# Kernel optimization log

Hardware: AMD Instinct MI355X
Metric: run time of the kernel (lower is better)

The kernel has to match this reference:

```python
import jax, jax.numpy as jnp
import numpy as np
import math

HIDDEN = 256
HEADS = 8
HEAD_DIM = HIDDEN // HEADS
SCALE = math.sqrt(HEAD_DIM)


def setup_inputs() -> dict:
    key = jax.random.key(0)
    ks = jax.random.split(key, 10)
    B, N = 2, 4096
    x = jax.random.normal(ks[0], (B, N, HIDDEN), dtype=jnp.float32)
    pos = jax.random.normal(ks[1], (B, N, 3), dtype=jnp.float32)
    s = 1.0 / math.sqrt(HIDDEN)
    Wq = jax.random.normal(ks[2], (HIDDEN, HIDDEN), dtype=jnp.float32) * s
    bq = jnp.zeros((HIDDEN,), dtype=jnp.float32)
    Wk = jax.random.normal(ks[3], (HIDDEN, HIDDEN), dtype=jnp.float32) * s
    bk = jnp.zeros((HIDDEN,), dtype=jnp.float32)
    Wv = jax.random.normal(ks[4], (HIDDEN, HIDDEN), dtype=jnp.float32) * s
    bv = jnp.zeros((HIDDEN,), dtype=jnp.float32)
    Wo = jax.random.normal(ks[5], (HIDDEN, HIDDEN), dtype=jnp.float32) * s
    bo = jnp.zeros((HIDDEN,), dtype=jnp.float32)
    return {"x": x, "pos": pos, "Wq": Wq, "bq": bq, "Wk": Wk, "bk": bk,
            "Wv": Wv, "bv": bv, "Wo": Wo, "bo": bo}


def _pairwise_dist(pos):
    # Euclidean cdist via the norm trick; clip for numerical safety.
    sq = jnp.sum(pos * pos, axis=-1)  # [B, N]
    d2 = sq[:, :, None] + sq[:, None, :] - 2.0 * jnp.einsum('bic,bjc->bij', pos, pos)
    return jnp.sqrt(jnp.maximum(d2, 0.0))  # [B, N, N]


def reference(x, pos, Wq, bq, Wk, bk, Wv, bv, Wo, bo):
    B, N, _ = x.shape
    # projections -> [B, H, N, Dh]
    def split_heads(t):
        return t.reshape(B, N, HEADS, HEAD_DIM).transpose(0, 2, 1, 3)
    q = split_heads(x @ Wq.T + bq)
    k = split_heads(x @ Wk.T + bk)
    v = split_heads(x @ Wv.T + bv)
    scores = jnp.einsum('bhid,bhjd->bhij', q, k) / SCALE
    dist_bias = -_pairwise_dist(pos) / 10.0  # [B, N, N]
    scores = scores + dist_bias[:, None, :, :]
    attn = jax.nn.softmax(scores, axis=-1)
    out = jnp.einsum('bhij,bhjd->bhid', attn, v)
    out = out.transpose(0, 2, 1, 3).reshape(B, N, HIDDEN)
    return out @ Wo.T + bo
```

## Files before the change

### kernel.cpp

```cpp
#include <hip/hip_runtime.h>

#define BATCH 2
#define SEQ   4096
#define HID   256
#define NHEAD 8
#define DH    32

typedef __attribute__((ext_vector_type(8))) _Float16 half8;
typedef __attribute__((ext_vector_type(4))) _Float16 half4;
typedef __attribute__((ext_vector_type(4))) float    f32x4;

__global__ void cvt_f32_f16(const float* __restrict__ src,
                            _Float16* __restrict__ dst, int n) {
    int i = (blockIdx.x * blockDim.x + threadIdx.x) * 4;
    if (i >= n) return;
    f32x4 v = *reinterpret_cast<const f32x4*>(src + i);
    half4 h;
#pragma unroll
    for (int c = 0; c < 4; ++c) h[c] = (_Float16)v[c];
    *reinterpret_cast<half4*>(dst + i) = h;
}

__global__ __launch_bounds__(256) void qkv_proj(
    const _Float16* __restrict__ xh, const _Float16* __restrict__ Wh,
    const float* __restrict__ bq, const float* __restrict__ bk,
    const float* __restrict__ bv,
    _Float16* __restrict__ Qh, _Float16* __restrict__ Kh,
    _Float16* __restrict__ Vt)
{
    const int z   = blockIdx.z;
    const int m0  = blockIdx.x * 64;
    const int n0  = blockIdx.y * 64;
    const int tid = threadIdx.x;
    const int w   = tid >> 6, lane = tid & 63;
    const int lr  = lane & 15, lg = lane >> 4;
    const int wr  = (w >> 1) * 32, wc = (w & 1) * 32;

    const _Float16* Wp = Wh + (size_t)z * HID * HID;
    const float* bias = (z == 0) ? bq : (z == 1) ? bk : bv;

    f32x4 acc[2][2] = {};
    const int ar = m0 + wr + lr;
    const int br = n0 + wc + lr;
#pragma unroll
    for (int ks = 0; ks < 8; ++ks) {
        const int ko = ks * 32 + lg * 8;
        half8 a0 = *reinterpret_cast<const half8*>(xh + (size_t)ar * HID + ko);
        half8 a1 = *reinterpret_cast<const half8*>(xh + (size_t)(ar + 16) * HID + ko);
        half8 b0 = *reinterpret_cast<const half8*>(Wp + (size_t)br * HID + ko);
        half8 b1 = *reinterpret_cast<const half8*>(Wp + (size_t)(br + 16) * HID + ko);
        acc[0][0] = __builtin_amdgcn_mfma_f32_16x16x32_f16(a0, b0, acc[0][0], 0, 0, 0);
        acc[0][1] = __builtin_amdgcn_mfma_f32_16x16x32_f16(a0, b1, acc[0][1], 0, 0, 0);
        acc[1][0] = __builtin_amdgcn_mfma_f32_16x16x32_f16(a1, b0, acc[1][0], 0, 0, 0);
        acc[1][1] = __builtin_amdgcn_mfma_f32_16x16x32_f16(a1, b1, acc[1][1], 0, 0, 0);
    }
#pragma unroll
    for (int mf = 0; mf < 2; ++mf)
#pragma unroll
    for (int nf = 0; nf < 2; ++nf)
#pragma unroll
    for (int r = 0; r < 4; ++r) {
        const int m  = m0 + wr + mf * 16 + lg * 4 + r;
        const int o  = n0 + wc + nf * 16 + lr;
        const int bb = m >> 12, nn = m & (SEQ - 1);
        const int hh = o >> 5,  dd = o & (DH - 1);
        float v = acc[mf][nf][r] + bias[o];
        if (z == 0) {
            Qh[(((size_t)(bb * NHEAD + hh) * SEQ) + nn) * DH + dd] =
                (_Float16)(v * 0.17677669529663687f);
        } else if (z == 1) {
            Kh[(((size_t)(bb * NHEAD + hh) * SEQ) + nn) * DH + dd] = (_Float16)v;
        } else {
            Vt[(((size_t)(bb * NHEAD + hh) * DH) + dd) * SEQ + nn] = (_Float16)v;
        }
    }
}

__global__ __launch_bounds__(512) void attn_kernel(
    const _Float16* __restrict__ Qh, const _Float16* __restrict__ Kh,
    const _Float16* __restrict__ Vt, const float* __restrict__ pos,
    _Float16* __restrict__ AO)
{
    __shared__ __align__(16) float pi[32][4];
    __shared__ __align__(16) float pj[64][4];
    __shared__ __align__(16) float sbias[32][68];
    __shared__ __align__(16) _Float16 Pl[NHEAD][2048];

    const int b   = blockIdx.y;
    const int i0  = blockIdx.x * 32;
    const int tid = threadIdx.x;
    const int h   = tid >> 6;
    const int lane = tid & 63;
    const int lr  = lane & 15, lg = lane >> 4;

    if (tid < 32) {
        const float* p = pos + (size_t)(b * SEQ + i0 + tid) * 3;
        float x = p[0], y = p[1], zz = p[2];
        pi[tid][0] = x; pi[tid][1] = y; pi[tid][2] = zz;
        pi[tid][3] = x * x + y * y + zz * zz;
    }

    const _Float16* Qbase = Qh + ((size_t)(b * NHEAD + h) * SEQ + i0) * DH;
    const _Float16* Kbase = Kh + (size_t)(b * NHEAD + h) * SEQ * DH;
    const _Float16* Vbase = Vt + (size_t)(b * NHEAD + h) * DH * SEQ;

    const half8 aq0 = *reinterpret_cast<const half8*>(Qbase + (size_t)lr * DH + lg * 8);
    const half8 aq1 = *reinterpret_cast<const half8*>(Qbase + (size_t)(16 + lr) * DH + lg * 8);

    f32x4 acc[2][2] = {};
    float mrun[2][4], lrun[2][4];
#pragma unroll
    for (int mf = 0; mf < 2; ++mf)
#pragma unroll
    for (int r = 0; r < 4; ++r) { mrun[mf][r] = -__builtin_inff(); lrun[mf][r] = 0.f; }

    char* Pbytes = (char*)&Pl[h][0];

    for (int jt = 0; jt < SEQ / 64; ++jt) {
        const int j0 = jt * 64;
        __syncthreads();
        if (tid < 64) {
            const float* p = pos + (size_t)(b * SEQ + j0 + tid) * 3;
            float x = p[0], y = p[1], zz = p[2];
            pj[tid][0] = x; pj[tid][1] = y; pj[tid][2] = zz;
            pj[tid][3] = x * x + y * y + zz * zz;
        }
        __syncthreads();
        {
            const int row = tid >> 4, c0 = (tid & 15) * 4;
            const float xi = pi[row][0], yi = pi[row][1], zi = pi[row][2], si = pi[row][3];
            f32x4 bb;
#pragma unroll
            for (int c = 0; c < 4; ++c) {
                const int col = c0 + c;
                float dot = xi * pj[col][0] + yi * pj[col][1] + zi * pj[col][2];
                float d2  = si + pj[col][3] - 2.f * dot;
                bb[c] = -0.1f * sqrtf(fmaxf(d2, 0.f));
            }
            *reinterpret_cast<f32x4*>(&sbias[row][c0]) = bb;
        }
        __syncthreads();

        half8 bk8[4];
#pragma unroll
        for (int cf = 0; cf < 4; ++cf)
            bk8[cf] = *reinterpret_cast<const half8*>(
                Kbase + (size_t)(j0 + cf * 16 + lr) * DH + lg * 8);
        f32x4 s[2][4];
#pragma unroll
        for (int mf = 0; mf < 2; ++mf)
#pragma unroll
        for (int cf = 0; cf < 4; ++cf) {
            f32x4 zero = {};
            s[mf][cf] = __builtin_amdgcn_mfma_f32_16x16x32_f16(
                mf ? aq1 : aq0, bk8[cf], zero, 0, 0, 0);
        }

#pragma unroll
        for (int mf = 0; mf < 2; ++mf)
#pragma unroll
        for (int r = 0; r < 4; ++r) {
            const int row = mf * 16 + lg * 4 + r;
            float v[4];
#pragma unroll
            for (int c = 0; c < 4; ++c) v[c] = s[mf][c][r] + sbias[row][c * 16 + lr];
            float tmax = fmaxf(fmaxf(v[0], v[1]), fmaxf(v[2], v[3]));
#pragma unroll
            for (int msk = 8; msk >= 1; msk >>= 1)
                tmax = fmaxf(tmax, __shfl_xor(tmax, msk, 64));
            const float mold = mrun[mf][r];
            const float mnew = fmaxf(mold, tmax);
            const float alpha = __expf(mold - mnew);
            float rsum = 0.f;
#pragma unroll
            for (int c = 0; c < 4; ++c) { v[c] = __expf(v[c] - mnew); rsum += v[c]; }
#pragma unroll
            for (int msk = 8; msk >= 1; msk >>= 1)
                rsum += __shfl_xor(rsum, msk, 64);
            lrun[mf][r] = lrun[mf][r] * alpha + rsum;
            mrun[mf][r] = mnew;
            acc[mf][0][r] *= alpha;
            acc[mf][1][r] *= alpha;
#pragma unroll
            for (int c = 0; c < 4; ++c) {
                const int col = c * 16 + lr;
                const int off = (row * 128 + col * 2) ^ ((row & 7) << 4);
                *reinterpret_cast<_Float16*>(Pbytes + off) = (_Float16)v[c];
            }
        }

#pragma unroll
        for (int ks = 0; ks < 2; ++ks) {
            half8 bv0 = *reinterpret_cast<const half8*>(
                Vbase + (size_t)lr * SEQ + j0 + ks * 32 + lg * 8);
            half8 bv1 = *reinterpret_cast<const half8*>(
                Vbase + (size_t)(16 + lr) * SEQ + j0 + ks * 32 + lg * 8);
#pragma unroll
            for (int mf = 0; mf < 2; ++mf) {
                const int prow = mf * 16 + lr;
                const int poff = (prow * 128 + (ks * 32 + lg * 8) * 2) ^ ((prow & 7) << 4);
                half8 pa = *reinterpret_cast<const half8*>(Pbytes + poff);
                acc[mf][0] = __builtin_amdgcn_mfma_f32_16x16x32_f16(pa, bv0, acc[mf][0], 0, 0, 0);
                acc[mf][1] = __builtin_amdgcn_mfma_f32_16x16x32_f16(pa, bv1, acc[mf][1], 0, 0, 0);
            }
        }
    }

#pragma unroll
    for (int mf = 0; mf < 2; ++mf)
#pragma unroll
    for (int r = 0; r < 4; ++r) {
        const float inv = 1.f / lrun[mf][r];
        const int row = mf * 16 + lg * 4 + r;
#pragma unroll
        for (int df = 0; df < 2; ++df) {
            AO[((size_t)(b * SEQ + i0 + row)) * HID + h * DH + df * 16 + lr] =
                (_Float16)(acc[mf][df][r] * inv);
        }
    }
}

__global__ __launch_bounds__(256) void out_proj(
    const _Float16* __restrict__ AO, const _Float16* __restrict__ Woh,
    const float* __restrict__ bo, float* __restrict__ out)
{
    const int m0  = blockIdx.x * 64;
    const int n0  = blockIdx.y * 64;
    const int tid = threadIdx.x;
    const int w   = tid >> 6, lane = tid & 63;
    const int lr  = lane & 15, lg = lane >> 4;
    const int wr  = (w >> 1) * 32, wc = (w & 1) * 32;

    f32x4 acc[2][2] = {};
    const int ar = m0 + wr + lr;
    const int br = n0 + wc + lr;
#pragma unroll
    for (int ks = 0; ks < 8; ++ks) {
        const int ko = ks * 32 + lg * 8;
        half8 a0 = *reinterpret_cast<const half8*>(AO + (size_t)ar * HID + ko);
        half8 a1 = *reinterpret_cast<const half8*>(AO + (size_t)(ar + 16) * HID + ko);
        half8 b0 = *reinterpret_cast<const half8*>(Woh + (size_t)br * HID + ko);
        half8 b1 = *reinterpret_cast<const half8*>(Woh + (size_t)(br + 16) * HID + ko);
        acc[0][0] = __builtin_amdgcn_mfma_f32_16x16x32_f16(a0, b0, acc[0][0], 0, 0, 0);
        acc[0][1] = __builtin_amdgcn_mfma_f32_16x16x32_f16(a0, b1, acc[0][1], 0, 0, 0);
        acc[1][0] = __builtin_amdgcn_mfma_f32_16x16x32_f16(a1, b0, acc[1][0], 0, 0, 0);
        acc[1][1] = __builtin_amdgcn_mfma_f32_16x16x32_f16(a1, b1, acc[1][1], 0, 0, 0);
    }
#pragma unroll
    for (int mf = 0; mf < 2; ++mf)
#pragma unroll
    for (int nf = 0; nf < 2; ++nf)
#pragma unroll
    for (int r = 0; r < 4; ++r) {
        const int m = m0 + wr + mf * 16 + lg * 4 + r;
        const int o = n0 + wc + nf * 16 + lr;
        out[(size_t)m * HID + o] = acc[mf][nf][r] + bo[o];
    }
}

extern "C" void kernel_launch(void* const* d_in, const int* in_sizes, int n_in,
                              void* d_out, int out_size, void* d_ws, size_t ws_size,
                              hipStream_t stream)
{
    const float* x   = (const float*)d_in[0];
    const float* pos = (const float*)d_in[1];
    const float* Wq  = (const float*)d_in[2];
    const float* bq  = (const float*)d_in[3];
    const float* Wk  = (const float*)d_in[4];
    const float* bk  = (const float*)d_in[5];
    const float* Wv  = (const float*)d_in[6];
    const float* bv  = (const float*)d_in[7];
    const float* Wo  = (const float*)d_in[8];
    const float* bo  = (const float*)d_in[9];
    float* out = (float*)d_out;

    char* ws = (char*)d_ws;
    _Float16* Qh = (_Float16*)(ws);
    _Float16* Kh = (_Float16*)(ws + (4  << 20));
    _Float16* Vt = (_Float16*)(ws + (8  << 20));
    _Float16* xh = (_Float16*)(ws + (12 << 20));
    _Float16* AO = xh;
    _Float16* Wh = (_Float16*)(ws + (16 << 20));

    const int NX = BATCH * SEQ * HID;
    const int NW = HID * HID;
    cvt_f32_f16<<<NX / 1024, 256, 0, stream>>>(x,  xh, NX);
    cvt_f32_f16<<<NW / 1024, 256, 0, stream>>>(Wq, Wh + 0 * NW, NW);
    cvt_f32_f16<<<NW / 1024, 256, 0, stream>>>(Wk, Wh + 1 * NW, NW);
    cvt_f32_f16<<<NW / 1024, 256, 0, stream>>>(Wv, Wh + 2 * NW, NW);
    cvt_f32_f16<<<NW / 1024, 256, 0, stream>>>(Wo, Wh + 3 * NW, NW);

    qkv_proj<<<dim3(BATCH * SEQ / 64, HID / 64, 3), 256, 0, stream>>>(
        xh, Wh, bq, bk, bv, Qh, Kh, Vt);

    attn_kernel<<<dim3(SEQ / 32, BATCH), 512, 0, stream>>>(Qh, Kh, Vt, pos, AO);

    out_proj<<<dim3(BATCH * SEQ / 64, HID / 64), 256, 0, stream>>>(
        AO, Wh + 3 * NW, bo, out);
}
```

Baseline: 287.8 us.

## Split attention keys across two wave groups with lazy rescale and merge

The attention block grows to 1024 threads, and each head is handled by two waves that each cover half of the key sequence. Their partial softmax states are merged through shared memory at the end. The online softmax skips rescaling unless a row max rises past a threshold, and row sums are reduced once at the end instead of every tile. The distance bias is computed for 128-key chunks in a transposed layout so it can be read as vectors, and the four weight conversions are folded into one launch. The change is meant to raise parallelism per block and cut the shuffle and exp overhead, at the cost of more shared memory, a final merge step, and a threshold that lets exponents grow.

Measured after the change: 327.0 us. 1.14x slower.

```diff
diff --git a/kernel.cpp b/kernel.cpp
--- a/kernel.cpp
+++ b/kernel.cpp
@@ -5,6 +5,7 @@
 #define HID   256
 #define NHEAD 8
 #define DH    32
+#define RESCALE_THR 8.0f
 
 typedef __attribute__((ext_vector_type(8))) _Float16 half8;
 typedef __attribute__((ext_vector_type(4))) _Float16 half4;
@@ -19,6 +20,19 @@
 #pragma unroll
     for (int c = 0; c < 4; ++c) h[c] = (_Float16)v[c];
     *reinterpret_cast<half4*>(dst + i) = h;
+}
+
+__global__ void cvt_w4(const float* __restrict__ a, const float* __restrict__ b,
+                       const float* __restrict__ c, const float* __restrict__ d,
+                       _Float16* __restrict__ dst) {
+    const float* srcs[4] = {a, b, c, d};
+    const float* s = srcs[blockIdx.y];
+    const int i = (blockIdx.x * blockDim.x + threadIdx.x) * 4;
+    f32x4 v = *reinterpret_cast<const f32x4*>(s + i);
+    half4 h;
+#pragma unroll
+    for (int k = 0; k < 4; ++k) h[k] = (_Float16)v[k];
+    *reinterpret_cast<half4*>(dst + (size_t)blockIdx.y * HID * HID + i) = h;
 }
 
 __global__ __launch_bounds__(256) void qkv_proj(
@@ -76,146 +90,198 @@
     }
 }
 
-__global__ __launch_bounds__(512) void attn_kernel(
+__global__ __launch_bounds__(1024, 4) void attn_kernel(
     const _Float16* __restrict__ Qh, const _Float16* __restrict__ Kh,
     const _Float16* __restrict__ Vt, const float* __restrict__ pos,
     _Float16* __restrict__ AO)
 {
     __shared__ __align__(16) float pi[32][4];
-    __shared__ __align__(16) float pj[64][4];
-    __shared__ __align__(16) float sbias[32][68];
-    __shared__ __align__(16) _Float16 Pl[NHEAD][2048];
-
-    const int b   = blockIdx.y;
-    const int i0  = blockIdx.x * 32;
-    const int tid = threadIdx.x;
-    const int h   = tid >> 6;
+    __shared__ __align__(16) float pj[2][128][4];
+    __shared__ __align__(16) float bias_t[2][128][33];
+    __shared__ __align__(16) _Float16 Pl[16][2048];
+
+    const int b    = blockIdx.y;
+    const int i0   = blockIdx.x * 32;
+    const int tid  = threadIdx.x;
+    const int w    = tid >> 6;
+    const int hh   = w & 7;
+    const int jh   = w >> 3;
     const int lane = tid & 63;
-    const int lr  = lane & 15, lg = lane >> 4;
+    const int lr   = lane & 15, lg = lane >> 4;
 
     if (tid < 32) {
         const float* p = pos + (size_t)(b * SEQ + i0 + tid) * 3;
-        float x = p[0], y = p[1], zz = p[2];
-        pi[tid][0] = x; pi[tid][1] = y; pi[tid][2] = zz;
-        pi[tid][3] = x * x + y * y + zz * zz;
-    }
-
-    const _Float16* Qbase = Qh + ((size_t)(b * NHEAD + h) * SEQ + i0) * DH;
-    const _Float16* Kbase = Kh + (size_t)(b * NHEAD + h) * SEQ * DH;
-    const _Float16* Vbase = Vt + (size_t)(b * NHEAD + h) * DH * SEQ;
+        float x = p[0], y = p[1], z = p[2];
+        pi[tid][0] = x; pi[tid][1] = y; pi[tid][2] = z;
+        pi[tid][3] = x * x + y * y + z * z;
+    }
+
+    const size_t bhh = (size_t)(b * NHEAD + hh);
+    const _Float16* Qbase = Qh + (bhh * SEQ + i0) * DH;
+    const _Float16* Kbase = Kh + bhh * SEQ * DH;
+    const _Float16* Vbase = Vt + bhh * DH * SEQ;
+    const int jbase = jh * (SEQ / 2);
 
     const half8 aq0 = *reinterpret_cast<const half8*>(Qbase + (size_t)lr * DH + lg * 8);
     const half8 aq1 = *reinterpret_cast<const half8*>(Qbase + (size_t)(16 + lr) * DH + lg * 8);
 
     f32x4 acc[2][2] = {};
-    float mrun[2][4], lrun[2][4];
-#pragma unroll
-    for (int mf = 0; mf < 2; ++mf)
-#pragma unroll
-    for (int r = 0; r < 4; ++r) { mrun[mf][r] = -__builtin_inff(); lrun[mf][r] = 0.f; }
-
-    char* Pbytes = (char*)&Pl[h][0];
-
-    for (int jt = 0; jt < SEQ / 64; ++jt) {
-        const int j0 = jt * 64;
+    float mrun[2][4], lsum[2][4];
+#pragma unroll
+    for (int mf = 0; mf < 2; ++mf)
+#pragma unroll
+    for (int r = 0; r < 4; ++r) { mrun[mf][r] = -__builtin_inff(); lsum[mf][r] = 0.f; }
+
+    char* Pbytes = (char*)&Pl[w][0];
+
+    for (int ch = 0; ch < 16; ++ch) {
+        const int c0 = ch * 128;
         __syncthreads();
-        if (tid < 64) {
-            const float* p = pos + (size_t)(b * SEQ + j0 + tid) * 3;
-            float x = p[0], y = p[1], zz = p[2];
-            pj[tid][0] = x; pj[tid][1] = y; pj[tid][2] = zz;
-            pj[tid][3] = x * x + y * y + zz * zz;
+        if (tid < 256) {
+            const int hf = tid >> 7, jc = tid & 127;
+            const float* p = pos + (size_t)(b * SEQ + hf * (SEQ / 2) + c0 + jc) * 3;
+            float x = p[0], y = p[1], z = p[2];
+            pj[hf][jc][0] = x; pj[hf][jc][1] = y; pj[hf][jc][2] = z;
+            pj[hf][jc][3] = x * x + y * y + z * z;
         }
         __syncthreads();
         {
-            const int row = tid >> 4, c0 = (tid & 15) * 4;
-            const float xi = pi[row][0], yi = pi[row][1], zi = pi[row][2], si = pi[row][3];
-            f32x4 bb;
-#pragma unroll
-            for (int c = 0; c < 4; ++c) {
-                const int col = c0 + c;
-                float dot = xi * pj[col][0] + yi * pj[col][1] + zi * pj[col][2];
-                float d2  = si + pj[col][3] - 2.f * dot;
-                bb[c] = -0.1f * sqrtf(fmaxf(d2, 0.f));
+            const int hf  = tid >> 9;
+            const int col = (tid >> 2) & 127;
+            const int r0  = (tid & 3) * 8;
+            const float xj = pj[hf][col][0], yj = pj[hf][col][1];
+            const float zj = pj[hf][col][2], sj = pj[hf][col][3];
+#pragma unroll
+            for (int r = 0; r < 8; ++r) {
+                const int row = r0 + r;
+                float dot = pi[row][0] * xj + pi[row][1] * yj + pi[row][2] * zj;
+                float d2  = pi[row][3] + sj - 2.f * dot;
+                bias_t[hf][col][row] = -0.1f * sqrtf(fmaxf(d2, 0.f));
             }
-            *reinterpret_cast<f32x4*>(&sbias[row][c0]) = bb;
         }
         __syncthreads();
 
-        half8 bk8[4];
-#pragma unroll
-        for (int cf = 0; cf < 4; ++cf)
-            bk8[cf] = *reinterpret_cast<const half8*>(
-                Kbase + (size_t)(j0 + cf * 16 + lr) * DH + lg * 8);
-        f32x4 s[2][4];
-#pragma unroll
-        for (int mf = 0; mf < 2; ++mf)
-#pragma unroll
-        for (int cf = 0; cf < 4; ++cf) {
-            f32x4 zero = {};
-            s[mf][cf] = __builtin_amdgcn_mfma_f32_16x16x32_f16(
-                mf ? aq1 : aq0, bk8[cf], zero, 0, 0, 0);
-        }
-
+#pragma unroll
+        for (int sub = 0; sub < 2; ++sub) {
+            const int jc0 = sub * 64;
+            const int j0  = jbase + c0 + jc0;
+
+            half8 bk8[4];
+#pragma unroll
+            for (int cf = 0; cf < 4; ++cf)
+                bk8[cf] = *reinterpret_cast<const half8*>(
+                    Kbase + (size_t)(j0 + cf * 16 + lr) * DH + lg * 8);
+
+#pragma unroll
+            for (int mf = 0; mf < 2; ++mf) {
+                float vv[4][4];
+#pragma unroll
+                for (int cf = 0; cf < 4; ++cf) {
+                    f32x4 zero = {};
+                    f32x4 sv = __builtin_amdgcn_mfma_f32_16x16x32_f16(
+                        mf ? aq1 : aq0, bk8[cf], zero, 0, 0, 0);
+                    f32x4 bb = *reinterpret_cast<const f32x4*>(
+                        &bias_t[jh][jc0 + cf * 16 + lr][mf * 16 + lg * 4]);
+#pragma unroll
+                    for (int r = 0; r < 4; ++r) vv[cf][r] = sv[r] + bb[r];
+                }
+                float tmax4[4];
+                int allok = 1;
+#pragma unroll
+                for (int r = 0; r < 4; ++r) {
+                    tmax4[r] = fmaxf(fmaxf(vv[0][r], vv[1][r]), fmaxf(vv[2][r], vv[3][r]));
+                    allok &= (tmax4[r] <= mrun[mf][r] + RESCALE_THR) ? 1 : 0;
+                }
+                if (!__all(allok)) {
+#pragma unroll
+                    for (int r = 0; r < 4; ++r) {
+                        float tm = tmax4[r];
+#pragma unroll
+                        for (int msk = 8; msk >= 1; msk >>= 1)
+                            tm = fmaxf(tm, __shfl_xor(tm, msk, 64));
+                        const float mnew  = fmaxf(mrun[mf][r], tm);
+                        const float alpha = __expf(mrun[mf][r] - mnew);
+                        lsum[mf][r] *= alpha;
+                        acc[mf][0][r] *= alpha;
+                        acc[mf][1][r] *= alpha;
+                        mrun[mf][r] = mnew;
+                    }
+                }
+#pragma unroll
+                for (int cf = 0; cf < 4; ++cf) {
+                    const int colb = (cf * 16 + lr) * 2;
+#pragma unroll
+                    for (int r = 0; r < 4; ++r) {
+                        const int row = mf * 16 + lg * 4 + r;
+                        const float p = __expf(vv[cf][r] - mrun[mf][r]);
+                        lsum[mf][r] += p;
+                        const int off = (row * 128 + colb) ^ ((row & 7) << 4);
+                        *reinterpret_cast<_Float16*>(Pbytes + off) = (_Float16)p;
+                    }
+                }
+            }
+
+#pragma unroll
+            for (int ks = 0; ks < 2; ++ks) {
+                half8 bv0 = *reinterpret_cast<const half8*>(
+                    Vbase + (size_t)lr * SEQ + j0 + ks * 32 + lg * 8);
+                half8 bv1 = *reinterpret_cast<const half8*>(
+                    Vbase + (size_t)(16 + lr) * SEQ + j0 + ks * 32 + lg * 8);
+#pragma unroll
+                for (int mf = 0; mf < 2; ++mf) {
+                    const int prow = mf * 16 + lr;
+                    const int poff = (prow * 128 + (ks * 32 + lg * 8) * 2) ^ ((prow & 7) << 4);
+                    half8 pa = *reinterpret_cast<const half8*>(Pbytes + poff);
+                    acc[mf][0] = __builtin_amdgcn_mfma_f32_16x16x32_f16(pa, bv0, acc[mf][0], 0, 0, 0);
+                    acc[mf][1] = __builtin_amdgcn_mfma_f32_16x16x32_f16(pa, bv1, acc[mf][1], 0, 0, 0);
+                }
+            }
+        }
+    }
+
+#pragma unroll
+    for (int mf = 0; mf < 2; ++mf)
+#pragma unroll
+    for (int r = 0; r < 4; ++r) {
+        float s = lsum[mf][r];
+#pragma unroll
+        for (int msk = 8; msk >= 1; msk >>= 1) s += __shfl_xor(s, msk, 64);
+        lsum[mf][r] = s;
+    }
+    __syncthreads();
+    float* accL = reinterpret_cast<float*>(&Pl[0][0]);
+    float* mlL  = reinterpret_cast<float*>(&bias_t[0][0][0]);
+#pragma unroll
+    for (int mf = 0; mf < 2; ++mf)
+#pragma unroll
+    for (int r = 0; r < 4; ++r) {
+        const int row = mf * 16 + lg * 4 + r;
+#pragma unroll
+        for (int df = 0; df < 2; ++df)
+            accL[(w * 32 + row) * 32 + df * 16 + lr] = acc[mf][df][r];
+        if (lr == 0) {
+            mlL[(w * 32 + row) * 2 + 0] = mrun[mf][r];
+            mlL[(w * 32 + row) * 2 + 1] = lsum[mf][r];
+        }
+    }
+    __syncthreads();
+    if (w < 8) {
 #pragma unroll
         for (int mf = 0; mf < 2; ++mf)
 #pragma unroll
         for (int r = 0; r < 4; ++r) {
             const int row = mf * 16 + lg * 4 + r;
-            float v[4];
-#pragma unroll
-            for (int c = 0; c < 4; ++c) v[c] = s[mf][c][r] + sbias[row][c * 16 + lr];
-            float tmax = fmaxf(fmaxf(v[0], v[1]), fmaxf(v[2], v[3]));
-#pragma unroll
-            for (int msk = 8; msk >= 1; msk >>= 1)
-                tmax = fmaxf(tmax, __shfl_xor(tmax, msk, 64));
-            const float mold = mrun[mf][r];
-            const float mnew = fmaxf(mold, tmax);
-            const float alpha = __expf(mold - mnew);
-            float rsum = 0.f;
-#pragma unroll
-            for (int c = 0; c < 4; ++c) { v[c] = __expf(v[c] - mnew); rsum += v[c]; }
-#pragma unroll
-            for (int msk = 8; msk >= 1; msk >>= 1)
-                rsum += __shfl_xor(rsum, msk, 64);
-            lrun[mf][r] = lrun[mf][r] * alpha + rsum;
-            mrun[mf][r] = mnew;
-            acc[mf][0][r] *= alpha;
-            acc[mf][1][r] *= alpha;
-#pragma unroll
-            for (int c = 0; c < 4; ++c) {
-                const int col = c * 16 + lr;
-                const int off = (row * 128 + col * 2) ^ ((row & 7) << 4);
-                *reinterpret_cast<_Float16*>(Pbytes + off) = (_Float16)v[c];
+            const float m0 = mlL[(w * 32 + row) * 2],       l0 = mlL[(w * 32 + row) * 2 + 1];
+            const float m1 = mlL[((w + 8) * 32 + row) * 2], l1 = mlL[((w + 8) * 32 + row) * 2 + 1];
+            const float mm = fmaxf(m0, m1);
+            const float e0 = __expf(m0 - mm), e1 = __expf(m1 - mm);
+            const float inv = 1.f / (l0 * e0 + l1 * e1);
+#pragma unroll
+            for (int df = 0; df < 2; ++df) {
+                const float o = (accL[(w * 32 + row) * 32 + df * 16 + lr] * e0 +
+                                 accL[((w + 8) * 32 + row) * 32 + df * 16 + lr] * e1) * inv;
+                AO[((size_t)(b * SEQ + i0 + row)) * HID + hh * DH + df * 16 + lr] = (_Float16)o;
             }
-        }
-
-#pragma unroll
-        for (int ks = 0; ks < 2; ++ks) {
-            half8 bv0 = *reinterpret_cast<const half8*>(
-                Vbase + (size_t)lr * SEQ + j0 + ks * 32 + lg * 8);
-            half8 bv1 = *reinterpret_cast<const half8*>(
-                Vbase + (size_t)(16 + lr) * SEQ + j0 + ks * 32 + lg * 8);
-#pragma unroll
-            for (int mf = 0; mf < 2; ++mf) {
-                const int prow = mf * 16 + lr;
-                const int poff = (prow * 128 + (ks * 32 + lg * 8) * 2) ^ ((prow & 7) << 4);
-                half8 pa = *reinterpret_cast<const half8*>(Pbytes + poff);
-                acc[mf][0] = __builtin_amdgcn_mfma_f32_16x16x32_f16(pa, bv0, acc[mf][0], 0, 0, 0);
-                acc[mf][1] = __builtin_amdgcn_mfma_f32_16x16x32_f16(pa, bv1, acc[mf][1], 0, 0, 0);
-            }
-        }
-    }
-
-#pragma unroll
-    for (int mf = 0; mf < 2; ++mf)
-#pragma unroll
-    for (int r = 0; r < 4; ++r) {
-        const float inv = 1.f / lrun[mf][r];
-        const int row = mf * 16 + lg * 4 + r;
-#pragma unroll
-        for (int df = 0; df < 2; ++df) {
-            AO[((size_t)(b * SEQ + i0 + row)) * HID + h * DH + df * 16 + lr] =
-                (_Float16)(acc[mf][df][r] * inv);
         }
     }
 }
@@ -284,16 +350,13 @@
 
     const int NX = BATCH * SEQ * HID;
     const int NW = HID * HID;
-    cvt_f32_f16<<<NX / 1024, 256, 0, stream>>>(x,  xh, NX);
-    cvt_f32_f16<<<NW / 1024, 256, 0, stream>>>(Wq, Wh + 0 * NW, NW);
-    cvt_f32_f16<<<NW / 1024, 256, 0, stream>>>(Wk, Wh + 1 * NW, NW);
-    cvt_f32_f16<<<NW / 1024, 256, 0, stream>>>(Wv, Wh + 2 * NW, NW);
-    cvt_f32_f16<<<NW / 1024, 256, 0, stream>>>(Wo, Wh + 3 * NW, NW);
+    cvt_f32_f16<<<NX / 1024, 256, 0, stream>>>(x, xh, NX);
+    cvt_w4<<<dim3(NW / 1024, 4), 256, 0, stream>>>(Wq, Wk, Wv, Wo, Wh);
 
     qkv_proj<<<dim3(BATCH * SEQ / 64, HID / 64, 3), 256, 0, stream>>>(
         xh, Wh, bq, bk, bv, Qh, Kh, Vt);
 
-    attn_kernel<<<dim3(SEQ / 32, BATCH), 512, 0, stream>>>(Qh, Kh, Vt, pos, AO);
+    attn_kernel<<<dim3(SEQ / 32, BATCH), 1024, 0, stream>>>(Qh, Kh, Vt, pos, AO);
 
     out_proj<<<dim3(BATCH * SEQ / 64, HID / 64), 256, 0, stream>>>(
         AO, Wh + 3 * NW, bo, out);
```
